# Optimization experiments

Measured on AMD Instinct MI355X. Metric: run time of the kernel, lower is better.

The kernel has to match this reference:

```python
import jax, jax.numpy as jnp
import numpy as np

B, T, H, N = 8, 1024, 256, 100
LOGITS_TEMP = 0.1
COS_EPS = 1e-8
NEG_FILL = -1e9


def setup_inputs() -> dict:
    key = jax.random.key(0)
    k1, k2, k3, k4 = jax.random.split(key, 4)
    return {
        "quantized_features": jax.random.normal(k1, (B, T, H), dtype=jnp.float32),
        "features": jax.random.normal(k2, (B, T, H), dtype=jnp.float32),
        "negative_indices": jax.random.randint(k3, (B, T * N), 0, B * T, dtype=jnp.int64),
        "mask_time_indices": jax.random.randint(k4, (B, T), 0, 2).astype(jnp.bool_),
    }


def _cosine_similarity(x, y, eps=COS_EPS):
    # torch.F.cosine_similarity semantics: dot / (max(|x|,eps)*max(|y|,eps))
    xn = jnp.maximum(jnp.linalg.norm(x, axis=-1), eps)
    yn = jnp.maximum(jnp.linalg.norm(y, axis=-1), eps)
    return jnp.sum(x * y, axis=-1) / (xn * yn)


def reference(quantized_features, features, negative_indices, mask_time_indices):
    b, t, h = quantized_features.shape
    n = negative_indices.shape[1] // t
    # gather negatives: (B*T, H)[idx] -> (B, T, N, H) -> (N, B, T, H)
    flat = quantized_features.reshape(-1, h)
    negs = flat[negative_indices.reshape(-1)].reshape(b, t, n, h).transpose(2, 0, 1, 3)
    # targets: positive first, then negatives -> (N+1, B, T, H)
    targets = jnp.concatenate([quantized_features[None], negs], axis=0)
    # cosine similarity against encoder output, broadcast over candidate dim
    logits = _cosine_similarity(features[None], targets) / LOGITS_TEMP  # (N+1, B, T)
    # mask out negatives identical to the positive
    neg_is_pos = jnp.all(quantized_features[None] == negs, axis=-1)  # (N, B, T)
    neg_is_pos = jnp.concatenate(
        [jnp.zeros((1, b, t), dtype=jnp.bool_), neg_is_pos], axis=0)
    logits = jnp.where(neg_is_pos, NEG_FILL, logits)
    # predictions: (T*B, N+1), label is always class 0 (the positive)
    preds = logits.transpose(2, 1, 0).reshape(-1, n + 1)
    logp = jax.nn.log_softmax(preds, axis=-1)
    ce = -logp[:, 0]  # CE with target 0
    # targets = -100 where unmasked -> zeroed by target_mask; sum reduction
    mask_flat = mask_time_indices.T.reshape(-1).astype(ce.dtype)  # matches transpose(1,0).flatten()
    return jnp.sum(ce * mask_flat)
```

## Files before the change

kernel.cpp:

```cpp
#include <hip/hip_runtime.h>
#include <math.h>

#define B_ 8
#define T_ 1024
#define H_ 256
#define N_ 100
#define NC_ 101
#define BT_ (B_ * T_)
#define GROUPS_ 16
#define COS_EPS_ 1e-8f
#define NEG_FILL_ -1e9f

#if defined(__has_builtin)
#if __has_builtin(__builtin_amdgcn_sdot4)
#define USE_I8 1
#else
#define USE_I8 0
#endif
#else
#define USE_I8 0
#endif

typedef _Float16 h2 __attribute__((ext_vector_type(2)));
typedef _Float16 h4 __attribute__((ext_vector_type(4)));

__device__ __forceinline__ float wredsum(float v) {
    v += __shfl_xor(v, 1);
    v += __shfl_xor(v, 2);
    v += __shfl_xor(v, 4);
    v += __shfl_xor(v, 8);
    v += __shfl_xor(v, 16);
    v += __shfl_xor(v, 32);
    return v;
}

__device__ __forceinline__ float wredmax(float v) {
    v = fmaxf(v, __shfl_xor(v, 1));
    v = fmaxf(v, __shfl_xor(v, 2));
    v = fmaxf(v, __shfl_xor(v, 4));
    v = fmaxf(v, __shfl_xor(v, 8));
    v = fmaxf(v, __shfl_xor(v, 16));
    v = fmaxf(v, __shfl_xor(v, 32));
    return v;
}

__device__ __forceinline__ h2 as_h2(unsigned u) {
    union { unsigned u; h2 h; } x;
    x.u = u;
    return x.h;
}

__device__ __forceinline__ float dot16(const uint4 a, const uint4 b, float acc) {
    acc = __builtin_amdgcn_fdot2(as_h2(a.x), as_h2(b.x), acc, false);
    acc = __builtin_amdgcn_fdot2(as_h2(a.y), as_h2(b.y), acc, false);
    acc = __builtin_amdgcn_fdot2(as_h2(a.z), as_h2(b.z), acc, false);
    acc = __builtin_amdgcn_fdot2(as_h2(a.w), as_h2(b.w), acc, false);
    return acc;
}

__device__ __forceinline__ unsigned pack4(const float4 v, const float r) {
    const int q0 = (int)rintf(v.x * r);
    const int q1 = (int)rintf(v.y * r);
    const int q2 = (int)rintf(v.z * r);
    const int q3 = (int)rintf(v.w * r);
    return (unsigned)(q0 & 255) | ((unsigned)(q1 & 255) << 8) |
           ((unsigned)(q2 & 255) << 16) | ((unsigned)(q3 & 255) << 24);
}

__global__ __launch_bounds__(256) void prep_kernel(
        const float* __restrict__ qf, const float* __restrict__ ff,
        unsigned char* __restrict__ q8, unsigned char* __restrict__ f8,
        _Float16* __restrict__ qh, _Float16* __restrict__ fh,
        float* __restrict__ sq, float* __restrict__ sf,
        const int* __restrict__ neg, const unsigned* __restrict__ mask,
        int* __restrict__ flags) {
    const int r = blockIdx.x * 4 + (threadIdx.x >> 6);
    const int lane = threadIdx.x & 63;
    const float4 q4 = ((const float4*)(qf + (size_t)r * H_))[lane];
    const float4 f4 = ((const float4*)(ff + (size_t)r * H_))[lane];
    const float qn = wredsum(q4.x * q4.x + q4.y * q4.y + q4.z * q4.z + q4.w * q4.w);
    const float fn = wredsum(f4.x * f4.x + f4.y * f4.y + f4.z * f4.z + f4.w * f4.w);
#if USE_I8
    float qm = fmaxf(fmaxf(fabsf(q4.x), fabsf(q4.y)), fmaxf(fabsf(q4.z), fabsf(q4.w)));
    float fm = fmaxf(fmaxf(fabsf(f4.x), fabsf(f4.y)), fmaxf(fabsf(f4.z), fabsf(f4.w)));
    qm = fmaxf(wredmax(qm), 1e-20f);
    fm = fmaxf(wredmax(fm), 1e-20f);
    ((unsigned*)(q8 + (size_t)r * H_))[lane] = pack4(q4, 127.0f / qm);
    ((unsigned*)(f8 + (size_t)r * H_))[lane] = pack4(f4, 127.0f / fm);
    if (lane == 0) {
        sq[r] = (qm / 127.0f) / fmaxf(sqrtf(qn), COS_EPS_);
        sf[r] = 10.0f * (fm / 127.0f) / fmaxf(sqrtf(fn), COS_EPS_);
    }
#else
    h4 hq = {(_Float16)q4.x, (_Float16)q4.y, (_Float16)q4.z, (_Float16)q4.w};
    h4 hf = {(_Float16)f4.x, (_Float16)f4.y, (_Float16)f4.z, (_Float16)f4.w};
    ((h4*)(qh + (size_t)r * H_))[lane] = hq;
    ((h4*)(fh + (size_t)r * H_))[lane] = hf;
    if (lane == 0) {
        sq[r] = 1.0f / fmaxf(sqrtf(qn), COS_EPS_);
        sf[r] = 10.0f / fmaxf(sqrtf(fn), COS_EPS_);
    }
#endif
    if (blockIdx.x == 0) {
        int ok_n = 1;
        int ok_m = 1;
        for (int i = threadIdx.x; i < 4096; i += 256) {
            if (neg[2 * i + 1] != 0) ok_n = 0;
        }
        for (int i = threadIdx.x; i < 2048; i += 256) {
            if (mask[i] > 1u) ok_m = 0;
        }
        const int rn = __syncthreads_and(ok_n);
        const int rm = __syncthreads_and(ok_m);
        if (threadIdx.x == 0) {
            flags[0] = rn;
            flags[1] = rm;
        }
    }
}

__global__ __launch_bounds__(256) void logits_kernel(
        const unsigned char* __restrict__ q8, const unsigned char* __restrict__ f8,
        const _Float16* __restrict__ qh, const _Float16* __restrict__ fh,
        const float* __restrict__ sq, const float* __restrict__ sf,
        const int* __restrict__ neg32, const void* __restrict__ maskp,
        const int* __restrict__ flags, float* __restrict__ ws_ce) {
    const int tid  = threadIdx.x;
    const int half = tid >> 7;
    const int hid  = tid & 127;
    const int g    = hid >> 3;
    const int sub  = tid & 7;
    const int bt   = blockIdx.x * 2 + half;
    const int shift = (flags[0] != 0) ? 1 : 0;
    const float sfb = sf[bt];

    float m = -INFINITY, s = 0.0f, logit0 = 0.0f;

#if USE_I8
    const uint4* frow = (const uint4*)(f8 + (size_t)bt * H_);
    const uint4 f0 = frow[sub], f1 = frow[sub + 8];
    for (int c = g; c < NC_; c += GROUPS_) {
        int row = bt;
        if (c > 0) {
            const long gi = (long)bt * N_ + (c - 1);
            row = neg32[gi << shift];
        }
        const uint4* cr = (const uint4*)(q8 + (size_t)row * H_);
        const uint4 c0 = cr[sub], c1 = cr[sub + 8];
        int ia = 0;
        ia = __builtin_amdgcn_sdot4((int)c0.x, (int)f0.x, ia, false);
        ia = __builtin_amdgcn_sdot4((int)c0.y, (int)f0.y, ia, false);
        ia = __builtin_amdgcn_sdot4((int)c0.z, (int)f0.z, ia, false);
        ia = __builtin_amdgcn_sdot4((int)c0.w, (int)f0.w, ia, false);
        ia = __builtin_amdgcn_sdot4((int)c1.x, (int)f1.x, ia, false);
        ia = __builtin_amdgcn_sdot4((int)c1.y, (int)f1.y, ia, false);
        ia = __builtin_amdgcn_sdot4((int)c1.z, (int)f1.z, ia, false);
        ia = __builtin_amdgcn_sdot4((int)c1.w, (int)f1.w, ia, false);
        ia += __shfl_xor(ia, 1);
        ia += __shfl_xor(ia, 2);
        ia += __shfl_xor(ia, 4);
        const float logit = ((c > 0) && (row == bt))
                                ? NEG_FILL_
                                : (float)ia * sfb * sq[row];
        if (c == 0) logit0 = logit;
        const float mn = fmaxf(m, logit);
        s = s * __expf(m - mn) + __expf(logit - mn);
        m = mn;
    }
#else
    const uint4* frow = (const uint4*)(fh + (size_t)bt * H_);
    const uint4 f0 = frow[sub], f1 = frow[sub + 8];
    const uint4 f2 = frow[sub + 16], f3 = frow[sub + 24];
    for (int c = g; c < NC_; c += GROUPS_) {
        int row = bt;
        if (c > 0) {
            const long gi = (long)bt * N_ + (c - 1);
            row = neg32[gi << shift];
        }
        const uint4* cr = (const uint4*)(qh + (size_t)row * H_);
        const uint4 c0 = cr[sub], c1 = cr[sub + 8];
        const uint4 c2 = cr[sub + 16], c3 = cr[sub + 24];
        float acc = dot16(c0, f0, 0.0f);
        acc = dot16(c1, f1, acc);
        acc = dot16(c2, f2, acc);
        acc = dot16(c3, f3, acc);
        acc += __shfl_xor(acc, 1);
        acc += __shfl_xor(acc, 2);
        acc += __shfl_xor(acc, 4);
        const float logit = ((c > 0) && (row == bt))
                                ? NEG_FILL_
                                : acc * sfb * sq[row];
        if (c == 0) logit0 = logit;
        const float mn = fmaxf(m, logit);
        s = s * __expf(m - mn) + __expf(logit - mn);
        m = mn;
    }
#endif

    __shared__ float sm_m[2][GROUPS_], sm_s[2][GROUPS_], sm_l0[2];
    if (sub == 0) {
        sm_m[half][g] = m;
        sm_s[half][g] = s;
        if (g == 0) sm_l0[half] = logit0;
    }
    __syncthreads();
    if (hid < GROUPS_) {
        const float mg = sm_m[half][hid];
        const float sg = sm_s[half][hid];
        float M = mg;
        M = fmaxf(M, __shfl_xor(M, 1));
        M = fmaxf(M, __shfl_xor(M, 2));
        M = fmaxf(M, __shfl_xor(M, 4));
        M = fmaxf(M, __shfl_xor(M, 8));
        float S = sg * __expf(mg - M);
        S += __shfl_xor(S, 1);
        S += __shfl_xor(S, 2);
        S += __shfl_xor(S, 4);
        S += __shfl_xor(S, 8);
        if (hid == 0) {
            const float ce = logf(S) + M - sm_l0[half];
            const bool mask32 = flags[1] != 0;
            const float mv = mask32 ? (float)((const int*)maskp)[bt]
                                    : (float)((const unsigned char*)maskp)[bt];
            ws_ce[bt] = ce * mv;
        }
    }
}

__global__ __launch_bounds__(256) void reduce_kernel(const float* __restrict__ ws_ce,
                                                     float* __restrict__ out) {
    __shared__ float sm[4];
    float s = 0.0f;
    for (int i = threadIdx.x; i < BT_; i += 256) s += ws_ce[i];
    s = wredsum(s);
    const int lane = threadIdx.x & 63, wave = threadIdx.x >> 6;
    if (lane == 0) sm[wave] = s;
    __syncthreads();
    if (threadIdx.x == 0) out[0] = sm[0] + sm[1] + sm[2] + sm[3];
}

extern "C" void kernel_launch(void* const* d_in, const int* in_sizes, int n_in,
                              void* d_out, int out_size, void* d_ws, size_t ws_size,
                              hipStream_t stream) {
    const float* qf  = (const float*)d_in[0];
    const float* ff  = (const float*)d_in[1];
    const int*   neg = (const int*)d_in[2];
    const void*  msk = d_in[3];

    char* p = (char*)d_ws;
    float* ws_ce = (float*)p; p += BT_ * sizeof(float);
    float* sq = (float*)p; p += BT_ * sizeof(float);
    float* sf = (float*)p; p += BT_ * sizeof(float);
    int* flags = (int*)p; p += 64;
    size_t off = (size_t)(p - (char*)d_ws);
    off = (off + 255) & ~(size_t)255;
    unsigned char* q8 = (unsigned char*)d_ws + off;
    unsigned char* f8 = q8 + (size_t)BT_ * H_;
    _Float16* qh = (_Float16*)(q8);
    _Float16* fh = qh + (size_t)BT_ * H_;

    prep_kernel<<<BT_ / 4, 256, 0, stream>>>(qf, ff, q8, f8, qh, fh, sq, sf,
                                             neg, (const unsigned*)msk, flags);
    logits_kernel<<<BT_ / 2, 256, 0, stream>>>(q8, f8, qh, fh, sq, sf,
                                               neg, msk, flags, ws_ce);
    reduce_kernel<<<1, 256, 0, stream>>>(ws_ce, (float*)d_out);
}
```

Before: 42.42 us.

## Skip unmasked rows and batch negative gathers with unrolled independent loads

Reads the time mask first and skips all gather and dot-product work for positions whose mask is zero, writing zero for them directly. The int8 path is restructured into a fully unrolled loop of 7 candidates: all indices are loaded first, then all candidate rows, then the dot products, then a single max and exp-sum pass replacing the online softmax. This removes about half the gather traffic and exposes more memory-level parallelism, at the cost of more registers. Note the fp16 fallback now sets logit0 when c == g, which differs from the original c == 0 condition. If any masked-out CE were NaN or inf, the result now differs from ce*0.

```diff
diff --git a/kernel.cpp b/kernel.cpp
--- a/kernel.cpp
+++ b/kernel.cpp
@@ -8,6 +8,7 @@
 #define NC_ 101
 #define BT_ (B_ * T_)
 #define GROUPS_ 16
+#define NITER_ 7
 #define COS_EPS_ 1e-8f
 #define NEG_FILL_ -1e9f
 
@@ -132,75 +133,86 @@
     const int sub  = tid & 7;
     const int bt   = blockIdx.x * 2 + half;
     const int shift = (flags[0] != 0) ? 1 : 0;
-    const float sfb = sf[bt];
-
-    float m = -INFINITY, s = 0.0f, logit0 = 0.0f;
-
+    const bool mask32 = flags[1] != 0;
+    const float mv = mask32 ? (float)((const int*)maskp)[bt]
+                            : (float)((const unsigned char*)maskp)[bt];
+
+    float Mt = -INFINITY, St = 0.0f, logit0 = 0.0f;
+
+    if (mv != 0.0f) {
 #if USE_I8
-    const uint4* frow = (const uint4*)(f8 + (size_t)bt * H_);
-    const uint4 f0 = frow[sub], f1 = frow[sub + 8];
-    for (int c = g; c < NC_; c += GROUPS_) {
-        int row = bt;
-        if (c > 0) {
-            const long gi = (long)bt * N_ + (c - 1);
-            row = neg32[gi << shift];
-        }
-        const uint4* cr = (const uint4*)(q8 + (size_t)row * H_);
-        const uint4 c0 = cr[sub], c1 = cr[sub + 8];
-        int ia = 0;
-        ia = __builtin_amdgcn_sdot4((int)c0.x, (int)f0.x, ia, false);
-        ia = __builtin_amdgcn_sdot4((int)c0.y, (int)f0.y, ia, false);
-        ia = __builtin_amdgcn_sdot4((int)c0.z, (int)f0.z, ia, false);
-        ia = __builtin_amdgcn_sdot4((int)c0.w, (int)f0.w, ia, false);
-        ia = __builtin_amdgcn_sdot4((int)c1.x, (int)f1.x, ia, false);
-        ia = __builtin_amdgcn_sdot4((int)c1.y, (int)f1.y, ia, false);
-        ia = __builtin_amdgcn_sdot4((int)c1.z, (int)f1.z, ia, false);
-        ia = __builtin_amdgcn_sdot4((int)c1.w, (int)f1.w, ia, false);
-        ia += __shfl_xor(ia, 1);
-        ia += __shfl_xor(ia, 2);
-        ia += __shfl_xor(ia, 4);
-        const float logit = ((c > 0) && (row == bt))
-                                ? NEG_FILL_
-                                : (float)ia * sfb * sq[row];
-        if (c == 0) logit0 = logit;
-        const float mn = fmaxf(m, logit);
-        s = s * __expf(m - mn) + __expf(logit - mn);
-        m = mn;
-    }
-#else
-    const uint4* frow = (const uint4*)(fh + (size_t)bt * H_);
-    const uint4 f0 = frow[sub], f1 = frow[sub + 8];
-    const uint4 f2 = frow[sub + 16], f3 = frow[sub + 24];
-    for (int c = g; c < NC_; c += GROUPS_) {
-        int row = bt;
-        if (c > 0) {
-            const long gi = (long)bt * N_ + (c - 1);
-            row = neg32[gi << shift];
-        }
-        const uint4* cr = (const uint4*)(qh + (size_t)row * H_);
-        const uint4 c0 = cr[sub], c1 = cr[sub + 8];
-        const uint4 c2 = cr[sub + 16], c3 = cr[sub + 24];
-        float acc = dot16(c0, f0, 0.0f);
-        acc = dot16(c1, f1, acc);
-        acc = dot16(c2, f2, acc);
-        acc = dot16(c3, f3, acc);
-        acc += __shfl_xor(acc, 1);
-        acc += __shfl_xor(acc, 2);
-        acc += __shfl_xor(acc, 4);
-        const float logit = ((c > 0) && (row == bt))
-                                ? NEG_FILL_
-                                : acc * sfb * sq[row];
-        if (c == 0) logit0 = logit;
-        const float mn = fmaxf(m, logit);
-        s = s * __expf(m - mn) + __expf(logit - mn);
-        m = mn;
-    }
-#endif
+        const uint4* frow = (const uint4*)(f8 + (size_t)bt * H_);
+        const uint4 f0 = frow[sub], f1 = frow[sub + 8];
+        int idx[NITER_];
+        #pragma unroll
+        for (int j = 0; j < NITER_; ++j) {
+            const int c = g + j * GROUPS_;
+            idx[j] = (c > 0 && c < NC_)
+                         ? neg32[((long)bt * N_ + (c - 1)) << shift]
+                         : bt;
+        }
+        uint4 r0[NITER_], r1[NITER_];
+        #pragma unroll
+        for (int j = 0; j < NITER_; ++j) {
+            const uint4* cr = (const uint4*)(q8 + (size_t)idx[j] * H_);
+            r0[j] = cr[sub];
+            r1[j] = cr[sub + 8];
+        }
+        const float sfb = sf[bt];
+        float lg[NITER_];
+        #pragma unroll
+        for (int j = 0; j < NITER_; ++j) {
+            int ia = 0;
+            ia = __builtin_amdgcn_sdot4((int)r0[j].x, (int)f0.x, ia, false);
+            ia = __builtin_amdgcn_sdot4((int)r0[j].y, (int)f0.y, ia, false);
+            ia = __builtin_amdgcn_sdot4((int)r0[j].z, (int)f0.z, ia, false);
+            ia = __builtin_amdgcn_sdot4((int)r0[j].w, (int)f0.w, ia, false);
+            ia = __builtin_amdgcn_sdot4((int)r1[j].x, (int)f1.x, ia, false);
+            ia = __builtin_amdgcn_sdot4((int)r1[j].y, (int)f1.y, ia, false);
+            ia = __builtin_amdgcn_sdot4((int)r1[j].z, (int)f1.z, ia, false);
+            ia = __builtin_amdgcn_sdot4((int)r1[j].w, (int)f1.w, ia, false);
+            ia += __shfl_xor(ia, 1);
+            ia += __shfl_xor(ia, 2);
+            ia += __shfl_xor(ia, 4);
+            const int c = g + j * GROUPS_;
+            const bool dead = (c >= NC_) || (c > 0 && idx[j] == bt);
+            lg[j] = dead ? NEG_FILL_ : (float)ia * sfb * sq[idx[j]];
+            if (c == 0) logit0 = lg[j];
+        }
+        #pragma unroll
+        for (int j = 0; j < NITER_; ++j) Mt = fmaxf(Mt, lg[j]);
+        #pragma unroll
+        for (int j = 0; j < NITER_; ++j) St += __expf(lg[j] - Mt);
+#else
+        const uint4* frow = (const uint4*)(fh + (size_t)bt * H_);
+        const uint4 f0 = frow[sub], f1 = frow[sub + 8];
+        const uint4 f2 = frow[sub + 16], f3 = frow[sub + 24];
+        for (int c = g; c < NC_; c += GROUPS_) {
+            int row = bt;
+            if (c > 0) row = neg32[((long)bt * N_ + (c - 1)) << shift];
+            const uint4* cr = (const uint4*)(qh + (size_t)row * H_);
+            float acc = dot16(cr[sub], f0, 0.0f);
+            acc = dot16(cr[sub + 8], f1, acc);
+            acc = dot16(cr[sub + 16], f2, acc);
+            acc = dot16(cr[sub + 24], f3, acc);
+            acc += __shfl_xor(acc, 1);
+            acc += __shfl_xor(acc, 2);
+            acc += __shfl_xor(acc, 4);
+            const float logit = ((c > 0) && (row == bt))
+                                    ? NEG_FILL_
+                                    : acc * sf[bt] * sq[row];
+            if (c == g) logit0 = logit;
+            const float mn = fmaxf(Mt, logit);
+            St = St * __expf(Mt - mn) + __expf(logit - mn);
+            Mt = mn;
+        }
+#endif
+    }
 
     __shared__ float sm_m[2][GROUPS_], sm_s[2][GROUPS_], sm_l0[2];
     if (sub == 0) {
-        sm_m[half][g] = m;
-        sm_s[half][g] = s;
+        sm_m[half][g] = Mt;
+        sm_s[half][g] = St;
         if (g == 0) sm_l0[half] = logit0;
     }
     __syncthreads();
@@ -219,10 +231,7 @@
         S += __shfl_xor(S, 8);
         if (hid == 0) {
             const float ce = logf(S) + M - sm_l0[half];
-            const bool mask32 = flags[1] != 0;
-            const float mv = mask32 ? (float)((const int*)maskp)[bt]
-                                    : (float)((const unsigned char*)maskp)[bt];
-            ws_ce[bt] = ce * mv;
+            ws_ce[bt] = (mv != 0.0f) ? ce * mv : 0.0f;
         }
     }
 }
```

Measured after the change: 40.68 us, median of 2. 1.04x faster.
